# Performance work log

Hardware: AMD Instinct MI355X
Metric: run time of the kernel (lower is better)

The kernel has to match this reference:

```python
import jax, jax.numpy as jnp
import numpy as np

NUM_BINS = 256


def setup_inputs() -> dict:
    key = jax.random.key(0)
    k1, k2 = jax.random.split(key)
    shape = (16, 3, 512, 512)
    I_complementary = jax.random.uniform(k1, shape, dtype=jnp.float32)
    I_target = jax.random.uniform(k2, shape, dtype=jnp.float32)
    return {"I_complementary": I_complementary, "I_target": I_target}


def reference(I_complementary, I_target):
    nb = NUM_BINS
    x = I_complementary.reshape(-1)
    y = I_target.reshape(-1)
    bx = jnp.clip(x * (nb - 1), 0, nb - 1).astype(jnp.int32)
    by = jnp.clip(y * (nb - 1), 0, nb - 1).astype(jnp.int32)
    # NOTE: torch's `hist[bx, by] += 1` is index_put WITHOUT accumulation, so
    # duplicate (bx,by) pairs all write old_value+1 = 1: the histogram is a
    # binary occupancy map, not counts. We replicate that with .at[].max(1).
    hist_2d = jnp.zeros((nb, nb), dtype=jnp.float32).at[bx, by].max(1.0)
    hist_2d = hist_2d / hist_2d.sum()
    p_x = hist_2d.sum(axis=1)  # [nb]
    p_y = hist_2d.sum(axis=0)  # [nb]
    mask = hist_2d > 0
    denom = p_x[:, None] * p_y[None, :] + 1e-10
    ratio = jnp.where(mask, hist_2d / denom, 1.0)
    mi = jnp.sum(jnp.where(mask, hist_2d * jnp.log(ratio), 0.0))
    return 1.0 - jnp.tanh(mi)
```

## Files before the change

### kernel.cpp

```cpp
#include <hip/hip_runtime.h>
#include <math.h>


#define NB 256
#define BM_WORDS 2048

__global__ void zero_bitmap_kernel(unsigned int* __restrict__ bm) {
    int i = blockIdx.x * blockDim.x + threadIdx.x;
    if (i < BM_WORDS) bm[i] = 0u;
}

__device__ __forceinline__ void set_bin(unsigned int* bm, float a, float b) {
    float va = fminf(fmaxf(a * 255.0f, 0.0f), 255.0f);
    float vb = fminf(fmaxf(b * 255.0f, 0.0f), 255.0f);
    int bx = (int)va;
    int by = (int)vb;
    int bin = (bx << 8) | by;
    atomicOr(&bm[bin >> 5], 1u << (bin & 31));
}

__global__ __launch_bounds__(512) void hist_kernel(const float* __restrict__ x,
                                                   const float* __restrict__ y,
                                                   unsigned int* __restrict__ gbm,
                                                   int n) {
    __shared__ unsigned int bm[BM_WORDS];
    for (int k = threadIdx.x; k < BM_WORDS; k += blockDim.x) bm[k] = 0u;
    __syncthreads();

    const int n4 = n >> 2;
    const float4* __restrict__ x4 = (const float4*)x;
    const float4* __restrict__ y4 = (const float4*)y;
    const int stride = gridDim.x * blockDim.x;
    for (int i = blockIdx.x * blockDim.x + threadIdx.x; i < n4; i += stride) {
        float4 a = x4[i];
        float4 b = y4[i];
        set_bin(bm, a.x, b.x);
        set_bin(bm, a.y, b.y);
        set_bin(bm, a.z, b.z);
        set_bin(bm, a.w, b.w);
    }
    for (int i = (n4 << 2) + blockIdx.x * blockDim.x + threadIdx.x; i < n; i += stride) {
        set_bin(bm, x[i], y[i]);
    }
    __syncthreads();

    for (int k = threadIdx.x; k < BM_WORDS; k += blockDim.x) {
        unsigned int v = bm[k];
        if (v) {
            unsigned int g = gbm[k];
            if (v & ~g) atomicOr(&gbm[k], v);
        }
    }
}

__global__ __launch_bounds__(256) void finalize_kernel(const unsigned int* __restrict__ gbm,
                                                       float* __restrict__ out) {
    __shared__ unsigned int w[BM_WORDS];
    __shared__ float rcs[NB];
    __shared__ float red[8];
    const int t = threadIdx.x;

    for (int k = t; k < BM_WORDS; k += 256) w[k] = gbm[k];
    __syncthreads();

    int r = 0;
#pragma unroll
    for (int k = 0; k < 8; ++k) r += __popc(w[t * 8 + k]);
    rcs[t] = (float)r;

    const int wsel = t >> 5;
    const int bsel = t & 31;
    int c = 0;
    for (int i = 0; i < NB; ++i) c += (w[i * 8 + wsel] >> bsel) & 1;
    __syncthreads();

    float S = 0.0f;
    for (int i = 0; i < NB; ++i) S += rcs[i];

    float partial = 0.0f;
    if (r > 0) partial += (float)r * logf((float)r / S);
    if (c > 0) partial += (float)c * logf((float)c / S);

    for (int off = 32; off > 0; off >>= 1) partial += __shfl_down(partial, off, 64);
    if ((t & 63) == 0) red[t >> 6] = partial;
    __syncthreads();
    if (t == 0) {
        float B = red[0] + red[1] + red[2] + red[3];
        float mi = -logf(S) - B / S;
        out[0] = 1.0f - tanhf(mi);
    }
}

extern "C" void kernel_launch(void* const* d_in, const int* in_sizes, int n_in,
                              void* d_out, int out_size, void* d_ws, size_t ws_size,
                              hipStream_t stream) {
    const float* x = (const float*)d_in[0];
    const float* y = (const float*)d_in[1];
    float* out = (float*)d_out;
    unsigned int* gbm = (unsigned int*)d_ws;
    const int n = in_sizes[0];

    zero_bitmap_kernel<<<(BM_WORDS + 255) / 256, 256, 0, stream>>>(gbm);
    hist_kernel<<<512, 512, 0, stream>>>(x, y, gbm, n);
    finalize_kernel<<<1, 256, 0, stream>>>(gbm, out);
}
```

Measured before the change: 137.9 us.

## Fuse finalize into histogram kernel via last-block ticket, unroll loads, double grid

Merges the finalize kernel into the histogram kernel: each block takes a ticket from an atomic counter, and the last block to finish reads the global bitmap and computes the mutual-information result. This removes one kernel launch and its launch gap. The main loop now issues three float4 pairs per iteration to raise memory-level parallelism. The grid grows from 512 to 1024 blocks with a launch bound of two blocks per CU. The cost is extra fence and atomic traffic, plus a serial tail on the last block.

```diff
diff --git a/kernel.cpp b/kernel.cpp
--- a/kernel.cpp
+++ b/kernel.cpp
@@ -5,84 +5,101 @@
 #define NB 256
 #define BM_WORDS 2048
 
-__global__ void zero_bitmap_kernel(unsigned int* __restrict__ bm) {
+__global__ void zero_kernel(unsigned int* __restrict__ bm) {
     int i = blockIdx.x * blockDim.x + threadIdx.x;
-    if (i < BM_WORDS) bm[i] = 0u;
+    if (i < BM_WORDS + 1) bm[i] = 0u;
 }
 
 __device__ __forceinline__ void set_bin(unsigned int* bm, float a, float b) {
     float va = fminf(fmaxf(a * 255.0f, 0.0f), 255.0f);
     float vb = fminf(fmaxf(b * 255.0f, 0.0f), 255.0f);
-    int bx = (int)va;
-    int by = (int)vb;
-    int bin = (bx << 8) | by;
+    int bin = ((int)va << 8) | (int)vb;
     atomicOr(&bm[bin >> 5], 1u << (bin & 31));
 }
 
-__global__ __launch_bounds__(512) void hist_kernel(const float* __restrict__ x,
-                                                   const float* __restrict__ y,
-                                                   unsigned int* __restrict__ gbm,
-                                                   int n) {
+__global__ __launch_bounds__(512, 2) void hist_kernel(const float* __restrict__ x,
+                                                      const float* __restrict__ y,
+                                                      unsigned int* __restrict__ gbm,
+                                                      float* __restrict__ out,
+                                                      int n) {
     __shared__ unsigned int bm[BM_WORDS];
-    for (int k = threadIdx.x; k < BM_WORDS; k += blockDim.x) bm[k] = 0u;
+    __shared__ float rcs[NB];
+    __shared__ float red[8];
+    __shared__ unsigned int ticket;
+    const int t = threadIdx.x;
+
+    for (int k = t; k < BM_WORDS; k += blockDim.x) bm[k] = 0u;
     __syncthreads();
 
     const int n4 = n >> 2;
     const float4* __restrict__ x4 = (const float4*)x;
     const float4* __restrict__ y4 = (const float4*)y;
-    const int stride = gridDim.x * blockDim.x;
-    for (int i = blockIdx.x * blockDim.x + threadIdx.x; i < n4; i += stride) {
-        float4 a = x4[i];
-        float4 b = y4[i];
-        set_bin(bm, a.x, b.x);
-        set_bin(bm, a.y, b.y);
-        set_bin(bm, a.z, b.z);
-        set_bin(bm, a.w, b.w);
+    const int nth = gridDim.x * blockDim.x;
+    int i = blockIdx.x * blockDim.x + t;
+
+    for (; i + 2 * nth < n4; i += 3 * nth) {
+        float4 a0 = x4[i];           float4 b0 = y4[i];
+        float4 a1 = x4[i + nth];     float4 b1 = y4[i + nth];
+        float4 a2 = x4[i + 2 * nth]; float4 b2 = y4[i + 2 * nth];
+        set_bin(bm, a0.x, b0.x); set_bin(bm, a0.y, b0.y);
+        set_bin(bm, a0.z, b0.z); set_bin(bm, a0.w, b0.w);
+        set_bin(bm, a1.x, b1.x); set_bin(bm, a1.y, b1.y);
+        set_bin(bm, a1.z, b1.z); set_bin(bm, a1.w, b1.w);
+        set_bin(bm, a2.x, b2.x); set_bin(bm, a2.y, b2.y);
+        set_bin(bm, a2.z, b2.z); set_bin(bm, a2.w, b2.w);
     }
-    for (int i = (n4 << 2) + blockIdx.x * blockDim.x + threadIdx.x; i < n; i += stride) {
-        set_bin(bm, x[i], y[i]);
+    for (; i < n4; i += nth) {
+        float4 a = x4[i]; float4 b = y4[i];
+        set_bin(bm, a.x, b.x); set_bin(bm, a.y, b.y);
+        set_bin(bm, a.z, b.z); set_bin(bm, a.w, b.w);
+    }
+    for (int j = (n4 << 2) + blockIdx.x * blockDim.x + t; j < n; j += nth) {
+        set_bin(bm, x[j], y[j]);
     }
     __syncthreads();
 
-    for (int k = threadIdx.x; k < BM_WORDS; k += blockDim.x) {
+    for (int k = t; k < BM_WORDS; k += blockDim.x) {
         unsigned int v = bm[k];
         if (v) {
             unsigned int g = gbm[k];
             if (v & ~g) atomicOr(&gbm[k], v);
         }
     }
-}
-
-__global__ __launch_bounds__(256) void finalize_kernel(const unsigned int* __restrict__ gbm,
-                                                       float* __restrict__ out) {
-    __shared__ unsigned int w[BM_WORDS];
-    __shared__ float rcs[NB];
-    __shared__ float red[8];
-    const int t = threadIdx.x;
-
-    for (int k = t; k < BM_WORDS; k += 256) w[k] = gbm[k];
     __syncthreads();
 
-    int r = 0;
+    if (t == 0) {
+        __threadfence();
+        ticket = __hip_atomic_fetch_add(&gbm[BM_WORDS], 1u, __ATOMIC_ACQ_REL,
+                                        __HIP_MEMORY_SCOPE_AGENT);
+    }
+    __syncthreads();
+    if (ticket != gridDim.x - 1) return;
+
+    __threadfence();
+    for (int k = t; k < BM_WORDS; k += blockDim.x)
+        bm[k] = __hip_atomic_load(&gbm[k], __ATOMIC_RELAXED, __HIP_MEMORY_SCOPE_AGENT);
+    __syncthreads();
+
+    float partial = 0.0f;
+    int r = 0, c = 0;
+    if (t < NB) {
 #pragma unroll
-    for (int k = 0; k < 8; ++k) r += __popc(w[t * 8 + k]);
-    rcs[t] = (float)r;
-
-    const int wsel = t >> 5;
-    const int bsel = t & 31;
-    int c = 0;
-    for (int i = 0; i < NB; ++i) c += (w[i * 8 + wsel] >> bsel) & 1;
+        for (int k = 0; k < 8; ++k) r += __popc(bm[t * 8 + k]);
+        rcs[t] = (float)r;
+        const int wsel = t >> 5;
+        const int bsel = t & 31;
+        for (int i2 = 0; i2 < NB; ++i2) c += (bm[i2 * 8 + wsel] >> bsel) & 1;
+    }
     __syncthreads();
 
     float S = 0.0f;
-    for (int i = 0; i < NB; ++i) S += rcs[i];
-
-    float partial = 0.0f;
-    if (r > 0) partial += (float)r * logf((float)r / S);
-    if (c > 0) partial += (float)c * logf((float)c / S);
-
-    for (int off = 32; off > 0; off >>= 1) partial += __shfl_down(partial, off, 64);
-    if ((t & 63) == 0) red[t >> 6] = partial;
+    if (t < NB) {
+        for (int i2 = 0; i2 < NB; ++i2) S += rcs[i2];
+        if (r > 0) partial += (float)r * logf((float)r / S);
+        if (c > 0) partial += (float)c * logf((float)c / S);
+        for (int off = 32; off > 0; off >>= 1) partial += __shfl_down(partial, off, 64);
+        if ((t & 63) == 0) red[t >> 6] = partial;
+    }
     __syncthreads();
     if (t == 0) {
         float B = red[0] + red[1] + red[2] + red[3];
@@ -100,7 +117,6 @@
     unsigned int* gbm = (unsigned int*)d_ws;
     const int n = in_sizes[0];
 
-    zero_bitmap_kernel<<<(BM_WORDS + 255) / 256, 256, 0, stream>>>(gbm);
-    hist_kernel<<<512, 512, 0, stream>>>(x, y, gbm, n);
-    finalize_kernel<<<1, 256, 0, stream>>>(gbm, out);
+    zero_kernel<<<(BM_WORDS + 1 + 255) / 256, 256, 0, stream>>>(gbm);
+    hist_kernel<<<1024, 512, 0, stream>>>(x, y, gbm, out, n);
 }
```

Result: slower. 185.4 us (+34.5%).
